# Optimization experiments

Measured on AMD Instinct MI355X. Metric: run time of the kernel, lower is better.

The kernel has to match this reference:

```python
import jax, jax.numpy as jnp
import numpy as np

N, E, FEAT, EMB, HID, V, EA, G = 10000, 250000, 16, 32, 32, 12, 9, 64
TEMP = 1.0


def setup_inputs() -> dict:
    key = jax.random.key(0)
    ks = jax.random.split(key, 20)
    p = lambda k, shp: jax.random.normal(k, shp, dtype=jnp.float32) * 0.05
    return {
        "x": jax.random.normal(ks[0], (N, FEAT), dtype=jnp.float32),
        "edge_attr": jax.random.normal(ks[1], (E, EA), dtype=jnp.float32),
        "edge_index": jax.random.randint(ks[2], (2, E), 0, N),
        "batch": jnp.sort(jax.random.randint(ks[3], (N,), 0, G)),
        # conv1 edge MLP: Linear(EA,32) -> ReLU -> Linear(32, FEAT*EMB)
        "nn1_w1": p(ks[4], (EA, 32)), "nn1_b1": p(ks[5], (32,)),
        "nn1_w2": p(ks[6], (32, FEAT * EMB)), "nn1_b2": p(ks[7], (FEAT * EMB,)),
        "root1": p(ks[8], (FEAT, EMB)), "bias1": p(ks[9], (EMB,)),
        # conv2 edge MLP: Linear(EA,32) -> ReLU -> Linear(32, EMB*HID)
        "nn2_w1": p(ks[10], (EA, 32)), "nn2_b1": p(ks[11], (32,)),
        "nn2_w2": p(ks[12], (32, EMB * HID)), "nn2_b2": p(ks[13], (EMB * HID,)),
        "root2": p(ks[14], (EMB, HID)), "bias2": p(ks[15], (HID,)),
        "lin_w": p(ks[16], (HID, V)), "lin_b": p(ks[17], (V,)),
    }


def _segment_mean(vals, ids, num_segments):
    s = jax.ops.segment_sum(vals, ids, num_segments=num_segments)
    cnt = jax.ops.segment_sum(jnp.ones((vals.shape[0],), vals.dtype), ids,
                              num_segments=num_segments)
    return s / jnp.maximum(cnt, 1.0)[:, None]


def _nnconv(h, edge_attr, src, dst, w1, b1, w2, b2, root, bias, din, dout):
    # edge MLP -> per-edge weight matrix [E, din, dout]
    we = (jax.nn.relu(edge_attr @ w1 + b1) @ w2 + b2).reshape(-1, din, dout)
    msg = jnp.einsum('ei,eio->eo', h[src], we)      # gather + per-edge matmul
    agg = _segment_mean(msg, dst, h.shape[0])       # scatter-mean to targets
    return agg + h @ root + bias                    # root weight + bias


def reference(x, edge_attr, edge_index, batch,
              nn1_w1, nn1_b1, nn1_w2, nn1_b2, root1, bias1,
              nn2_w1, nn2_b1, nn2_w2, nn2_b2, root2, bias2,
              lin_w, lin_b):
    src, dst = edge_index[0], edge_index[1]
    h = jax.nn.relu(_nnconv(x, edge_attr, src, dst,
                            nn1_w1, nn1_b1, nn1_w2, nn1_b2, root1, bias1,
                            FEAT, EMB))
    h = jax.nn.relu(_nnconv(h, edge_attr, src, dst,
                            nn2_w1, nn2_b1, nn2_w2, nn2_b2, root2, bias2,
                            EMB, HID))
    pooled = _segment_mean(h, batch, G)             # global_mean_pool [G, HID]
    logits = (pooled @ lin_w + lin_b) / TEMP
    return jax.nn.log_softmax(logits, axis=1)
```

## Files before the change

kernel.cpp:

```cpp
#include <hip/hip_runtime.h>
#include <hip/hip_bf16.h>
#include <stdint.h>

#define NN 10000
#define NE 250000
#define FEAT 16
#define EMB 32
#define HID 32
#define NV 12
#define EAD 9
#define NG 64
#define EPB 128
#define NCH 25

__device__ __forceinline__ uint32_t bf16rne(float f) {
    uint32_t u = __float_as_uint(f);
    return (u + 0x7fffu + ((u >> 16) & 1u)) >> 16;
}
__device__ __forceinline__ float blo(uint32_t p) { return __uint_as_float(p << 16); }
__device__ __forceinline__ float bhi(uint32_t p) { return __uint_as_float(p & 0xffff0000u); }

__global__ void edge_stats_kernel(const int* __restrict__ src,
                                  const int* __restrict__ dst,
                                  int* __restrict__ histS,
                                  int* __restrict__ histD) {
    int e = blockIdx.x * blockDim.x + threadIdx.x;
    if (e >= NE) return;
    atomicAdd(&histS[src[e]], 1);
    atomicAdd(&histD[dst[e]], 1);
}

__global__ __launch_bounds__(1024) void scan_kernel(const int* __restrict__ histS,
                                                    const int* __restrict__ histD,
                                                    int* __restrict__ rowS,
                                                    int* __restrict__ rowD,
                                                    int* __restrict__ curS,
                                                    int* __restrict__ curD) {
    const int* hist = blockIdx.x ? histD : histS;
    int* rowStart   = blockIdx.x ? rowD : rowS;
    int* cursor     = blockIdx.x ? curD : curS;
    __shared__ int part[1024];
    int t = threadIdx.x;
    int base = t * 10;
    int local[10];
    int s = 0;
#pragma unroll
    for (int i = 0; i < 10; ++i) {
        int v = (base + i < NN) ? hist[base + i] : 0;
        local[i] = s;
        s += v;
    }
    part[t] = s;
    __syncthreads();
    for (int off = 1; off < 1024; off <<= 1) {
        int v = (t >= off) ? part[t - off] : 0;
        __syncthreads();
        part[t] += v;
        __syncthreads();
    }
    int pre = (t == 0) ? 0 : part[t - 1];
#pragma unroll
    for (int i = 0; i < 10; ++i) {
        if (base + i < NN) {
            int rs = pre + local[i];
            rowStart[base + i] = rs;
            cursor[base + i] = rs;
        }
    }
    if (t == 1023) rowStart[NN] = part[1023];
}

__global__ void scatter_kernel(const float* __restrict__ ea,
                               const int* __restrict__ src,
                               const int* __restrict__ dst,
                               int* __restrict__ cursorS,
                               int* __restrict__ cursorD,
                               float* __restrict__ ea_p,
                               int* __restrict__ src_s,
                               int* __restrict__ perm_d) {
    int e = blockIdx.x * blockDim.x + threadIdx.x;
    if (e >= NE) return;
    int sv = src[e], dv = dst[e];
    int pos  = atomicAdd(&cursorS[sv], 1);
    int posd = atomicAdd(&cursorD[dv], 1);
    src_s[pos] = sv;
    perm_d[pos] = posd;
#pragma unroll
    for (int j = 0; j < 12; ++j)
        ea_p[(size_t)pos * 12 + j] = (j < EAD) ? ea[(size_t)e * EAD + j] : 0.f;
}

template <int DIN>
__global__ __launch_bounds__(256) void computeQ_pack_kernel(
    const float* __restrict__ h,
    const float* __restrict__ w2,
    uint32_t* __restrict__ Qp)
{
    int t = threadIdx.x;
    int o = t & 31;
    int kk = (blockIdx.y * 256 + t) >> 5;
    float w0[DIN], w1r[DIN];
    const float* wa = w2 + (size_t)(2 * kk) * (DIN * 32) + o;
    const float* wb = w2 + (size_t)(2 * kk + 1) * (DIN * 32) + o;
#pragma unroll
    for (int i = 0; i < DIN; ++i) { w0[i] = wa[i * 32]; w1r[i] = wb[i * 32]; }

    int n0 = blockIdx.x * NCH;
    for (int j = 0; j < NCH; ++j) {
        int n = n0 + j;
        const float* hn = h + (size_t)n * DIN;
        float s0 = 0.f, s1 = 0.f;
#pragma unroll
        for (int i = 0; i < DIN; ++i) {
            float hv = hn[i];
            s0 += hv * w0[i];
            s1 += hv * w1r[i];
        }
        Qp[((size_t)n * 16 + kk) * 32 + o] = (bf16rne(s1) << 16) | bf16rne(s0);
    }
}

template <int DIN>
__global__ void computeQbias_kernel(const float* __restrict__ h,
                                    const float* __restrict__ b2,
                                    float* __restrict__ Qb) {
    int idx = blockIdx.x * blockDim.x + threadIdx.x;
    if (idx >= NN * 32) return;
    int o = idx & 31;
    int n = idx >> 5;
    const float* hn = h + (size_t)n * DIN;
    float s = 0.f;
#pragma unroll
    for (int i = 0; i < DIN; ++i) s += hn[i] * b2[i * 32 + o];
    Qb[idx] = s;
}

__global__ __launch_bounds__(256) void edge_msg_kernel(
    const float* __restrict__ ea_p,
    const int* __restrict__ src_s,
    const int* __restrict__ perm_d,
    const float* __restrict__ w1,
    const float* __restrict__ b1,
    const uint32_t* __restrict__ Qp,
    const float* __restrict__ Qb,
    float* __restrict__ msg)
{
    __shared__ float s_hid[8][32];
    int t = threadIdx.x;
    int o = t & 31;
    int slot = t >> 5;

    float w1r[12];
#pragma unroll
    for (int j = 0; j < 12; ++j) w1r[j] = (j < EAD) ? w1[j * 32 + o] : 0.f;
    float b1r = b1[o];

    int base = blockIdx.x * EPB;
    int eend = min(base + EPB, NE);
    for (int e = base + slot; e < eend; e += 8) {
        const float4* eav = (const float4*)(ea_p + (size_t)e * 12);
        float4 a0 = eav[0], a1 = eav[1], a2 = eav[2];
        float hs = b1r;
        hs += a0.x * w1r[0] + a0.y * w1r[1] + a0.z * w1r[2] + a0.w * w1r[3];
        hs += a1.x * w1r[4] + a1.y * w1r[5] + a1.z * w1r[6] + a1.w * w1r[7];
        hs += a2.x * w1r[8];
        float hd = fmaxf(hs, 0.f);

        s_hid[slot][o] = hd;
        __builtin_amdgcn_wave_barrier();

        int sv = src_s[e];
        const uint32_t* q = Qp + (size_t)sv * 512 + o;
        float m = Qb[(size_t)sv * 32 + o];
        const float4* hq = (const float4*)(&s_hid[slot][0]);
#pragma unroll
        for (int c = 0; c < 8; ++c) {
            float4 hv = hq[c];
            uint32_t qa = q[(2 * c) * 32];
            uint32_t qb2 = q[(2 * c + 1) * 32];
            m += hv.x * blo(qa) + hv.y * bhi(qa)
               + hv.z * blo(qb2) + hv.w * bhi(qb2);
        }
        msg[(size_t)perm_d[e] * 32 + o] = m;
        __builtin_amdgcn_wave_barrier();
    }
}

template <int DIN>
__global__ __launch_bounds__(256) void aggregate_kernel(
    const float* __restrict__ msg,
    const int* __restrict__ dRow,
    const float* __restrict__ hin,
    const float* __restrict__ root,
    const float* __restrict__ bias,
    float* __restrict__ hout,
    float* __restrict__ pooled,
    const int* __restrict__ batch,
    float* __restrict__ gcnt)
{
    int t = threadIdx.x;
    int o = t & 31;
    int n = blockIdx.x * 8 + (t >> 5);
    int beg = dRow[n], end = dRow[n + 1];
    float s = 0.f;
    for (int r = beg; r < end; ++r) s += msg[(size_t)r * 32 + o];
    s /= fmaxf((float)(end - beg), 1.0f);
    s += bias[o];
    const float* h = hin + (size_t)n * DIN;
#pragma unroll
    for (int i = 0; i < DIN; ++i) s += h[i] * root[i * 32 + o];
    s = fmaxf(s, 0.f);
    hout[(size_t)n * 32 + o] = s;
    if (pooled) {
        int g = batch[n];
        atomicAdd(&pooled[g * 32 + o], s);
        if (o == 0) atomicAdd(&gcnt[g], 1.0f);
    }
}

__global__ void final_kernel(const float* __restrict__ pooled,
                             const float* __restrict__ gcnt,
                             const float* __restrict__ lin_w,
                             const float* __restrict__ lin_b,
                             float* __restrict__ out) {
    int g = threadIdx.x;
    if (g >= NG) return;
    float inv = 1.0f / fmaxf(gcnt[g], 1.0f);
    float p[HID];
#pragma unroll
    for (int h = 0; h < HID; ++h) p[h] = pooled[g * HID + h] * inv;
    float logits[NV];
    float mx = -1e30f;
#pragma unroll
    for (int v = 0; v < NV; ++v) {
        float s = lin_b[v];
#pragma unroll
        for (int h = 0; h < HID; ++h) s += p[h] * lin_w[h * NV + v];
        logits[v] = s;
        mx = fmaxf(mx, s);
    }
    float se = 0.f;
#pragma unroll
    for (int v = 0; v < NV; ++v) se += expf(logits[v] - mx);
    float lse = mx + logf(se);
#pragma unroll
    for (int v = 0; v < NV; ++v) out[g * NV + v] = logits[v] - lse;
}

extern "C" void kernel_launch(void* const* d_in, const int* in_sizes, int n_in,
                              void* d_out, int out_size, void* d_ws, size_t ws_size,
                              hipStream_t stream) {
    const float* x        = (const float*)d_in[0];
    const float* ea       = (const float*)d_in[1];
    const int*   eidx     = (const int*)d_in[2];
    const int*   batch    = (const int*)d_in[3];
    const float* nn1_w1   = (const float*)d_in[4];
    const float* nn1_b1   = (const float*)d_in[5];
    const float* nn1_w2   = (const float*)d_in[6];
    const float* nn1_b2   = (const float*)d_in[7];
    const float* root1    = (const float*)d_in[8];
    const float* bias1    = (const float*)d_in[9];
    const float* nn2_w1   = (const float*)d_in[10];
    const float* nn2_b1   = (const float*)d_in[11];
    const float* nn2_w2   = (const float*)d_in[12];
    const float* nn2_b2   = (const float*)d_in[13];
    const float* root2    = (const float*)d_in[14];
    const float* bias2    = (const float*)d_in[15];
    const float* lin_w    = (const float*)d_in[16];
    const float* lin_b    = (const float*)d_in[17];
    float* out = (float*)d_out;

    const int* src = eidx;
    const int* dst = eidx + NE;

    char* base = (char*)d_ws;
    uint32_t* Qp   = (uint32_t*)base;
    float* msg     = (float*)(Qp + (size_t)NN * 512);
    float* ea_p    = msg + (size_t)NE * 32;
    float* Qb      = ea_p + (size_t)NE * 12;
    float* h1      = Qb + (size_t)NN * 32;
    float* h2      = h1 + (size_t)NN * 32;
    int*   src_s   = (int*)(h2 + (size_t)NN * 32);
    int*   perm_d  = src_s + NE;
    int*   rowS    = perm_d + NE;
    int*   rowD    = rowS + NN + 1;
    int*   curS    = rowD + NN + 1;
    int*   curD    = curS + NN;
    int*   histS   = curD + NN;
    int*   histD   = histS + NN;
    float* pooled  = (float*)(histD + NN);
    float* gcnt    = pooled + NG * 32;
    size_t zero_bytes = ((size_t)NN * 2 + NG * 32 + NG) * 4;

    hipMemsetAsync(histS, 0, zero_bytes, stream);

    edge_stats_kernel<<<(NE + 255) / 256, 256, 0, stream>>>(src, dst, histS, histD);
    scan_kernel<<<2, 1024, 0, stream>>>(histS, histD, rowS, rowD, curS, curD);
    scatter_kernel<<<(NE + 255) / 256, 256, 0, stream>>>(ea, src, dst, curS, curD,
                                                         ea_p, src_s, perm_d);

    const int edge_grid = (NE + EPB - 1) / EPB;
    dim3 qgrid(NN / NCH, 2);

    computeQ_pack_kernel<FEAT><<<qgrid, 256, 0, stream>>>(x, nn1_w2, Qp);
    computeQbias_kernel<FEAT><<<(NN * 32) / 256, 256, 0, stream>>>(x, nn1_b2, Qb);
    edge_msg_kernel<<<edge_grid, 256, 0, stream>>>(ea_p, src_s, perm_d,
                                                   nn1_w1, nn1_b1, Qp, Qb, msg);
    aggregate_kernel<FEAT><<<NN / 8, 256, 0, stream>>>(
        msg, rowD, x, root1, bias1, h1, nullptr, nullptr, nullptr);

    computeQ_pack_kernel<EMB><<<qgrid, 256, 0, stream>>>(h1, nn2_w2, Qp);
    computeQbias_kernel<EMB><<<(NN * 32) / 256, 256, 0, stream>>>(h1, nn2_b2, Qb);
    edge_msg_kernel<<<edge_grid, 256, 0, stream>>>(ea_p, src_s, perm_d,
                                                   nn2_w1, nn2_b1, Qp, Qb, msg);
    aggregate_kernel<EMB><<<NN / 8, 256, 0, stream>>>(
        msg, rowD, h1, root2, bias2, h2, pooled, batch, gcnt);

    final_kernel<<<1, 64, 0, stream>>>(pooled, gcnt, lin_w, lin_b, out);
}
```

Baseline: 299.5 us.

## Replace dst-CSR message buffer with atomic scatter-add aggregation

Removes the per-edge message buffer (NE x 32 floats) and the destination CSR sort. Each edge's message is now atomically added straight into a per-node aggregation buffer, and node updates divide by the in-degree histogram. This cuts the large msg write/read traffic plus the dst scan and cursor atomics. In exchange it issues 250k x 32 float atomics per layer, needs an extra memset between layers, and makes the summation order nondeterministic.

```diff
diff --git a/kernel.cpp b/kernel.cpp
--- a/kernel.cpp
+++ b/kernel.cpp
@@ -30,15 +30,9 @@
     atomicAdd(&histD[dst[e]], 1);
 }
 
-__global__ __launch_bounds__(1024) void scan_kernel(const int* __restrict__ histS,
-                                                    const int* __restrict__ histD,
-                                                    int* __restrict__ rowS,
-                                                    int* __restrict__ rowD,
-                                                    int* __restrict__ curS,
-                                                    int* __restrict__ curD) {
-    const int* hist = blockIdx.x ? histD : histS;
-    int* rowStart   = blockIdx.x ? rowD : rowS;
-    int* cursor     = blockIdx.x ? curD : curS;
+__global__ __launch_bounds__(1024) void scan_kernel(const int* __restrict__ hist,
+                                                    int* __restrict__ rowStart,
+                                                    int* __restrict__ cursor) {
     __shared__ int part[1024];
     int t = threadIdx.x;
     int base = t * 10;
@@ -74,17 +68,15 @@
                                const int* __restrict__ src,
                                const int* __restrict__ dst,
                                int* __restrict__ cursorS,
-                               int* __restrict__ cursorD,
                                float* __restrict__ ea_p,
                                int* __restrict__ src_s,
-                               int* __restrict__ perm_d) {
+                               int* __restrict__ dst_s) {
     int e = blockIdx.x * blockDim.x + threadIdx.x;
     if (e >= NE) return;
-    int sv = src[e], dv = dst[e];
-    int pos  = atomicAdd(&cursorS[sv], 1);
-    int posd = atomicAdd(&cursorD[dv], 1);
+    int sv = src[e];
+    int pos = atomicAdd(&cursorS[sv], 1);
     src_s[pos] = sv;
-    perm_d[pos] = posd;
+    dst_s[pos] = dst[e];
 #pragma unroll
     for (int j = 0; j < 12; ++j)
         ea_p[(size_t)pos * 12 + j] = (j < EAD) ? ea[(size_t)e * EAD + j] : 0.f;
@@ -135,15 +127,15 @@
     Qb[idx] = s;
 }
 
-__global__ __launch_bounds__(256) void edge_msg_kernel(
+__global__ __launch_bounds__(256) void edge_agg_kernel(
     const float* __restrict__ ea_p,
     const int* __restrict__ src_s,
-    const int* __restrict__ perm_d,
+    const int* __restrict__ dst_s,
     const float* __restrict__ w1,
     const float* __restrict__ b1,
     const uint32_t* __restrict__ Qp,
     const float* __restrict__ Qb,
-    float* __restrict__ msg)
+    float* __restrict__ agg)
 {
     __shared__ float s_hid[8][32];
     int t = threadIdx.x;
@@ -176,41 +168,37 @@
 #pragma unroll
         for (int c = 0; c < 8; ++c) {
             float4 hv = hq[c];
-            uint32_t qa = q[(2 * c) * 32];
+            uint32_t qa  = q[(2 * c) * 32];
             uint32_t qb2 = q[(2 * c + 1) * 32];
             m += hv.x * blo(qa) + hv.y * bhi(qa)
                + hv.z * blo(qb2) + hv.w * bhi(qb2);
         }
-        msg[(size_t)perm_d[e] * 32 + o] = m;
+        atomicAdd(&agg[(size_t)dst_s[e] * 32 + o], m);
         __builtin_amdgcn_wave_barrier();
     }
 }
 
 template <int DIN>
-__global__ __launch_bounds__(256) void aggregate_kernel(
-    const float* __restrict__ msg,
-    const int* __restrict__ dRow,
-    const float* __restrict__ hin,
-    const float* __restrict__ root,
-    const float* __restrict__ bias,
-    float* __restrict__ hout,
-    float* __restrict__ pooled,
-    const int* __restrict__ batch,
-    float* __restrict__ gcnt)
+__global__ void node_update_kernel(const float* __restrict__ agg,
+                                   const int* __restrict__ histD,
+                                   const float* __restrict__ hin,
+                                   const float* __restrict__ root,
+                                   const float* __restrict__ bias,
+                                   float* __restrict__ hout,
+                                   float* __restrict__ pooled,
+                                   const int* __restrict__ batch,
+                                   float* __restrict__ gcnt)
 {
-    int t = threadIdx.x;
-    int o = t & 31;
-    int n = blockIdx.x * 8 + (t >> 5);
-    int beg = dRow[n], end = dRow[n + 1];
-    float s = 0.f;
-    for (int r = beg; r < end; ++r) s += msg[(size_t)r * 32 + o];
-    s /= fmaxf((float)(end - beg), 1.0f);
-    s += bias[o];
+    int idx = blockIdx.x * blockDim.x + threadIdx.x;
+    if (idx >= NN * 32) return;
+    int o = idx & 31;
+    int n = idx >> 5;
+    float s = bias[o] + agg[idx] / fmaxf((float)histD[n], 1.0f);
     const float* h = hin + (size_t)n * DIN;
 #pragma unroll
     for (int i = 0; i < DIN; ++i) s += h[i] * root[i * 32 + o];
     s = fmaxf(s, 0.f);
-    hout[(size_t)n * 32 + o] = s;
+    hout[idx] = s;
     if (pooled) {
         int g = batch[n];
         atomicAdd(&pooled[g * 32 + o], s);
@@ -275,46 +263,45 @@
 
     char* base = (char*)d_ws;
     uint32_t* Qp   = (uint32_t*)base;
-    float* msg     = (float*)(Qp + (size_t)NN * 512);
-    float* ea_p    = msg + (size_t)NE * 32;
+    float* ea_p    = (float*)(Qp + (size_t)NN * 512);
     float* Qb      = ea_p + (size_t)NE * 12;
     float* h1      = Qb + (size_t)NN * 32;
     float* h2      = h1 + (size_t)NN * 32;
     int*   src_s   = (int*)(h2 + (size_t)NN * 32);
-    int*   perm_d  = src_s + NE;
-    int*   rowS    = perm_d + NE;
-    int*   rowD    = rowS + NN + 1;
-    int*   curS    = rowD + NN + 1;
-    int*   curD    = curS + NN;
-    int*   histS   = curD + NN;
+    int*   dst_s   = src_s + NE;
+    int*   rowS    = dst_s + NE;
+    int*   curS    = rowS + NN + 1;
+    int*   histS   = curS + NN;
     int*   histD   = histS + NN;
     float* pooled  = (float*)(histD + NN);
     float* gcnt    = pooled + NG * 32;
-    size_t zero_bytes = ((size_t)NN * 2 + NG * 32 + NG) * 4;
+    float* agg     = gcnt + NG;
+    size_t zero_bytes = ((size_t)NN * 2 + NG * 32 + NG + (size_t)NN * 32) * 4;
 
     hipMemsetAsync(histS, 0, zero_bytes, stream);
 
     edge_stats_kernel<<<(NE + 255) / 256, 256, 0, stream>>>(src, dst, histS, histD);
-    scan_kernel<<<2, 1024, 0, stream>>>(histS, histD, rowS, rowD, curS, curD);
-    scatter_kernel<<<(NE + 255) / 256, 256, 0, stream>>>(ea, src, dst, curS, curD,
-                                                         ea_p, src_s, perm_d);
+    scan_kernel<<<1, 1024, 0, stream>>>(histS, rowS, curS);
+    scatter_kernel<<<(NE + 255) / 256, 256, 0, stream>>>(ea, src, dst, curS,
+                                                         ea_p, src_s, dst_s);
 
     const int edge_grid = (NE + EPB - 1) / EPB;
     dim3 qgrid(NN / NCH, 2);
 
     computeQ_pack_kernel<FEAT><<<qgrid, 256, 0, stream>>>(x, nn1_w2, Qp);
     computeQbias_kernel<FEAT><<<(NN * 32) / 256, 256, 0, stream>>>(x, nn1_b2, Qb);
-    edge_msg_kernel<<<edge_grid, 256, 0, stream>>>(ea_p, src_s, perm_d,
-                                                   nn1_w1, nn1_b1, Qp, Qb, msg);
-    aggregate_kernel<FEAT><<<NN / 8, 256, 0, stream>>>(
-        msg, rowD, x, root1, bias1, h1, nullptr, nullptr, nullptr);
-
+    edge_agg_kernel<<<edge_grid, 256, 0, stream>>>(ea_p, src_s, dst_s,
+                                                   nn1_w1, nn1_b1, Qp, Qb, agg);
+    node_update_kernel<FEAT><<<(NN * 32) / 256, 256, 0, stream>>>(
+        agg, histD, x, root1, bias1, h1, nullptr, nullptr, nullptr);
+
+    hipMemsetAsync(agg, 0, (size_t)NN * 32 * sizeof(float), stream);
     computeQ_pack_kernel<EMB><<<qgrid, 256, 0, stream>>>(h1, nn2_w2, Qp);
     computeQbias_kernel<EMB><<<(NN * 32) / 256, 256, 0, stream>>>(h1, nn2_b2, Qb);
-    edge_msg_kernel<<<edge_grid, 256, 0, stream>>>(ea_p, src_s, perm_d,
-                                                   nn2_w1, nn2_b1, Qp, Qb, msg);
-    aggregate_kernel<EMB><<<NN / 8, 256, 0, stream>>>(
-        msg, rowD, h1, root2, bias2, h2, pooled, batch, gcnt);
+    edge_agg_kernel<<<edge_grid, 256, 0, stream>>>(ea_p, src_s, dst_s,
+                                                   nn2_w1, nn2_b1, Qp, Qb, agg);
+    node_update_kernel<EMB><<<(NN * 32) / 256, 256, 0, stream>>>(
+        agg, histD, h1, root2, bias2, h2, pooled, batch, gcnt);
 
     final_kernel<<<1, 64, 0, stream>>>(pooled, gcnt, lin_w, lin_b, out);
 }
```

Result: faster. 279.2 us (-6.8%).
